# Optimization experiments

Measured on AMD Instinct MI355X. Metric: run time of the kernel, lower is better.

Reference implementation:

```python
import jax, jax.numpy as jnp
import numpy as np

BIG_CONST = 1000000.0
LN_EPS = 1e-5

B, S, D = 2, 1024, 1024
N, H = 16, D // 16            # n_head, d_head
POS_LEN = 2 * S - 1


def setup_inputs() -> dict:
    key = jax.random.key(0)
    ks = jax.random.split(key, 16)
    std_qkv = np.sqrt(1.0 / float(D + N * H))   # EinsumLayer init: 1/sqrt(fan_in+fan_out)
    std_post = np.sqrt(1.0 / float(N * H + D))
    return {
        "q": jax.random.normal(ks[0], (B, S, D), jnp.float32),
        "k": jax.random.normal(ks[1], (B, S, D), jnp.float32),
        "v": jax.random.normal(ks[2], (B, S, D), jnp.float32),
        "pos_enc": jax.random.normal(ks[3], (POS_LEN, D), jnp.float32),
        "attn_mask": jax.random.randint(ks[4], (B, 1, 1, S), 0, 2, jnp.int32),
        "q_w": jax.random.normal(ks[5], (D, N, H), jnp.float32) * std_qkv,
        "k_w": jax.random.normal(ks[6], (D, N, H), jnp.float32) * std_qkv,
        "k_b": jnp.zeros((N, H), jnp.float32),
        "v_w": jax.random.normal(ks[7], (D, N, H), jnp.float32) * std_qkv,
        "v_b": jnp.zeros((N, H), jnp.float32),
        "r_w_bias": jax.random.uniform(ks[8], (N, 1, H), jnp.float32, 0.0, 0.1),
        "r_r_bias": jax.random.uniform(ks[9], (N, 1, H), jnp.float32, 0.0, 0.1),
        "r_kernel": jax.random.uniform(ks[10], (N, D, H), jnp.float32, 0.0, 0.1),
        "post_w": jax.random.normal(ks[11], (N, H, D), jnp.float32) * std_post,
        "post_b": jnp.zeros((D,), jnp.float32),
        "ln_g": jnp.ones((D,), jnp.float32),
        "ln_b": jnp.zeros((D,), jnp.float32),
    }


def reference(q, k, v, pos_enc, attn_mask, q_w, k_w, k_b, v_w, v_b,
              r_w_bias, r_r_bias, r_kernel, post_w, post_b, ln_g, ln_b):
    input_q = q
    d_head = q_w.shape[-1]
    normalizer = 1.0 / np.sqrt(d_head)

    # head projections -> [B, N, L, H]
    qh = jnp.einsum('bld,dnh->bnlh', q, q_w)
    kh = jnp.einsum('bld,dnh->bnlh', k, k_w) + k_b[None, :, None, :] * 0 + jnp.transpose(k_b, (0, 1))[None, :, None, :] * 0 + k_b.reshape(1, k_b.shape[0], 1, k_b.shape[1])
    kh = jnp.einsum('bld,dnh->bnlh', k, k_w) + k_b.reshape(1, -1, 1, d_head)
    vh = jnp.einsum('bld,dnh->bnlh', v, v_w) + v_b.reshape(1, -1, 1, d_head)

    # content score: (q + r_w_bias) @ k^T * normalizer   [B,N,S,S]
    content = jnp.einsum('bnqh,bnkh->bnqk', qh + r_w_bias[None], kh) * normalizer

    # positional term (rel_shift with shift=0): r = pos_enc @ r_kernel -> [N, P, H]
    r = jnp.einsum('pd,ndh->nph', pos_enc, r_kernel)
    pos_scores = jnp.einsum('bnqh,nph->bnqp', qh + r_r_bias[None], r) * normalizer
    # shift=0 => reshape-swap + narrow + reshape-back is an exact identity; then narrow to k_len
    k_len = kh.shape[-2]
    pos_term = pos_scores[..., :k_len]

    attn_score = (content + pos_term).astype(jnp.float32)
    attn_score = attn_score - BIG_CONST * attn_mask.astype(jnp.float32)
    attn_dist = jax.nn.softmax(attn_score, axis=-1)

    out = jnp.einsum('bnqk,bnkh->bnqh', attn_dist, vh)          # [B,N,S,H]
    attn_out = jnp.einsum('bnlh,nhd->bld', out, post_w) + post_b

    x = input_q + attn_out
    mu = jnp.mean(x, axis=-1, keepdims=True)
    var = jnp.mean(jnp.square(x - mu), axis=-1, keepdims=True)
    return (x - mu) / jnp.sqrt(var + LN_EPS) * ln_g + ln_b
```

## Files before the change

### kernel.cpp

```cpp
#include <hip/hip_runtime.h>
#include <cstddef>
#include <cstdint>

typedef unsigned short u16;
typedef unsigned int   u32;

#define S_LEN  1024
#define NHEAD  16
#define HDIM   64
#define DMODEL 1024
#define NORMSC 0.125f
#define BIGC   1000000.0f
#define LOG2E  1.44269504088896f
#define SC2    (0.125f * 1.44269504088896f)

typedef __bf16 bf16x8 __attribute__((ext_vector_type(8)));
typedef float  f32x4  __attribute__((ext_vector_type(4)));

#define MFMA16(a, b, c) __builtin_amdgcn_mfma_f32_16x16x32_bf16((a), (b), (c), 0, 0, 0)

__device__ __forceinline__ u16 f2bf(float f) {
    u32 u = __float_as_uint(f);
    u32 r = (u + 0x7fffu + ((u >> 16) & 1u)) >> 16;
    return (u16)r;
}
__device__ __forceinline__ float bf2f(u32 v) {
    return __uint_as_float(v << 16);
}
__device__ __forceinline__ float4 unp4(uint2 u) {
    float4 f;
    f.x = bf2f(u.x & 0xffffu); f.y = bf2f(u.x >> 16);
    f.z = bf2f(u.y & 0xffffu); f.w = bf2f(u.y >> 16);
    return f;
}
__device__ __forceinline__ void async16(const void* g, void* l) {
    __builtin_amdgcn_global_load_lds(
        (__attribute__((address_space(1))) void*)(g),
        (__attribute__((address_space(3))) void*)(l), 16, 0, 0);
}

__global__ __launch_bounds__(256) void prep_all(
    const float* q, const float* k, const float* v, const float* pos,
    const float* qw, const float* kw, const float* vw, const float* pw, const float* rk,
    u16* qbf, u16* kbf, u16* vbf, u16* posb,
    u16* qwT, u16* kwT, u16* vwT, u16* pwT, u16* WrT)
{
    __shared__ float tb[32][33];
    const int bid = blockIdx.x, tid = threadIdx.x;
    if (bid < 7168) {
        const float* s; u16* d; int base;
        if (bid < 2048)      { s = q;   d = qbf;  base = bid; }
        else if (bid < 4096) { s = k;   d = kbf;  base = bid - 2048; }
        else if (bid < 6144) { s = v;   d = vbf;  base = bid - 4096; }
        else                 { s = pos; d = posb; base = bid - 6144; }
        const int i = base * 1024 + tid * 4;
        const float4 val = *(const float4*)&s[i];
        uint2 o;
        o.x = (u32)f2bf(val.x) | ((u32)f2bf(val.y) << 16);
        o.y = (u32)f2bf(val.z) | ((u32)f2bf(val.w) << 16);
        *(uint2*)&d[i] = o;
        return;
    }
    const int t = bid - 7168;
    const float* in; u16* out; int ild, r0, c0;
    if (t < 4096) {
        const int ts = t & 1023;
        if (t < 1024)      { in = qw; out = qwT; }
        else if (t < 2048) { in = kw; out = kwT; }
        else if (t < 3072) { in = vw; out = vwT; }
        else               { in = pw; out = pwT; }
        ild = 1024;
        r0 = (ts >> 5) * 32; c0 = (ts & 31) * 32;
    } else {
        const int ts = t - 4096;
        const int n = ts >> 6, tt = ts & 63;
        in = rk + (size_t)n * 65536; out = WrT + (size_t)n * 65536;
        ild = 64;
        r0 = (tt >> 1) * 32; c0 = (tt & 1) * 32;
    }
    const int tx = tid & 31, ty = tid >> 5;
    for (int i = ty; i < 32; i += 8)
        tb[i][tx] = in[(size_t)(r0 + i) * ild + c0 + tx];
    __syncthreads();
    for (int i = ty; i < 32; i += 8)
        out[(size_t)(c0 + i) * 1024 + r0 + tx] = f2bf(tb[tx][i]);
}

struct GJ { const u16* A; const u16* Bt; u16* C; int M; int k0; int klen; };

__global__ __launch_bounds__(256) void gemm_p(
    GJ j0, GJ j1, GJ j2, GJ j3, GJ j4, GJ j5, GJ j6, GJ j7)
{
    GJ g;
    switch (blockIdx.z) {
        case 0: g = j0; break; case 1: g = j1; break;
        case 2: g = j2; break; case 3: g = j3; break;
        case 4: g = j4; break; case 5: g = j5; break;
        case 6: g = j6; break; default: g = j7;
    }
    const int bm = blockIdx.y * 128;
    if (bm >= g.M) return;
    const int bn = blockIdx.x * 128;
    __shared__ u16 As[2][4096];
    __shared__ u16 Bs[2][4096];
    const int tid = threadIdx.x;
    const int w = tid >> 6, lane = tid & 63;
    const int wm = (w >> 1) * 64, wn = (w & 1) * 64;
    const int l15 = lane & 15, l16 = lane >> 4;
    f32x4 acc[4][4] = {};
    const char* Ab = (const char*)g.A;
    const char* Bb = (const char*)g.Bt;
    const int kend = g.k0 + g.klen;
    const int m0 = w * 1024 + lane * 16;
    const int m1 = (4 + w) * 1024 + lane * 16;
    const int r0w = m0 >> 6, cb0 = m0 & 63;
    const int r1w = m1 >> 6, cb1 = m1 & 63;
    async16(Ab + ((size_t)(bm + r0w) * 1024 + g.k0) * 2 + cb0, (char*)As[0] + m0);
    async16(Bb + ((size_t)(bn + r0w) * 1024 + g.k0) * 2 + cb0, (char*)Bs[0] + m0);
    async16(Ab + ((size_t)(bm + r1w) * 1024 + g.k0) * 2 + cb1, (char*)As[0] + m1);
    async16(Bb + ((size_t)(bn + r1w) * 1024 + g.k0) * 2 + cb1, (char*)Bs[0] + m1);
    int buf = 0;
    for (int k0 = g.k0; k0 < kend; k0 += 32) {
        __syncthreads();
        const int kn = k0 + 32;
        if (kn < kend) {
            async16(Ab + ((size_t)(bm + r0w) * 1024 + kn) * 2 + cb0, (char*)As[buf ^ 1] + m0);
            async16(Bb + ((size_t)(bn + r0w) * 1024 + kn) * 2 + cb0, (char*)Bs[buf ^ 1] + m0);
            async16(Ab + ((size_t)(bm + r1w) * 1024 + kn) * 2 + cb1, (char*)As[buf ^ 1] + m1);
            async16(Bb + ((size_t)(bn + r1w) * 1024 + kn) * 2 + cb1, (char*)Bs[buf ^ 1] + m1);
        }
        bf16x8 af[4], bfr[4];
#pragma unroll
        for (int i = 0; i < 4; ++i)
            af[i] = *(const bf16x8*)&As[buf][(wm + i * 16 + l15) * 32 + l16 * 8];
#pragma unroll
        for (int j = 0; j < 4; ++j)
            bfr[j] = *(const bf16x8*)&Bs[buf][(wn + j * 16 + l15) * 32 + l16 * 8];
#pragma unroll
        for (int i = 0; i < 4; ++i)
#pragma unroll
            for (int j = 0; j < 4; ++j)
                acc[i][j] = MFMA16(af[i], bfr[j], acc[i][j]);
        buf ^= 1;
    }
#pragma unroll
    for (int i = 0; i < 4; ++i)
#pragma unroll
        for (int j = 0; j < 4; ++j) {
            const int c = bn + wn + j * 16 + l15;
#pragma unroll
            for (int rg = 0; rg < 4; ++rg) {
                const int m = bm + wm + i * 16 + l16 * 4 + rg;
                g.C[(size_t)m * 1024 + c] = f2bf(acc[i][j][rg]);
            }
        }
}

__global__ __launch_bounds__(256) void prep2(
    const u16* pk0, const u16* pk1, const u16* pr0, const u16* pr1,
    const u16* pv0, const u16* pv1, const u16* pq0, const u16* pq1,
    const float* kbi, const float* vbi, const float* rwb, const float* rrb,
    const int* mask, u16* keff, float* cc, u16* vT, u16* qhb)
{
    __shared__ float tb[32][33];
    const int bid = blockIdx.x, tid = threadIdx.x;
    if (bid < 2048) {
        const int t = bid * 256 + tid;
        const int row = t >> 4, li = t & 15;
        const int n = (row >> 10) & 15, kk = row & 1023, b = row >> 14;
        const size_t mi = ((size_t)(b * 1024 + kk)) * 1024 + n * 64 + li * 4;
        const size_t pi = ((size_t)kk) * 1024 + n * 64 + li * 4;
        const float4 k0v = unp4(*(const uint2*)&pk0[mi]);
        const float4 k1v = unp4(*(const uint2*)&pk1[mi]);
        const float4 r0v = unp4(*(const uint2*)&pr0[pi]);
        const float4 r1v = unp4(*(const uint2*)&pr1[pi]);
        const float4 kb4 = *(const float4*)&kbi[n * 64 + li * 4];
        float4 kv, rv;
        kv.x = k0v.x + k1v.x + kb4.x; kv.y = k0v.y + k1v.y + kb4.y;
        kv.z = k0v.z + k1v.z + kb4.z; kv.w = k0v.w + k1v.w + kb4.w;
        rv.x = r0v.x + r1v.x; rv.y = r0v.y + r1v.y;
        rv.z = r0v.z + r1v.z; rv.w = r0v.w + r1v.w;
        const float4 w1 = *(const float4*)&rwb[n * 64 + li * 4];
        const float4 w2 = *(const float4*)&rrb[n * 64 + li * 4];
        float s = w1.x * kv.x + w1.y * kv.y + w1.z * kv.z + w1.w * kv.w
                + w2.x * rv.x + w2.y * rv.y + w2.z * rv.z + w2.w * rv.w;
        uint2 o;
        o.x = (u32)f2bf(kv.x + rv.x) | ((u32)f2bf(kv.y + rv.y) << 16);
        o.y = (u32)f2bf(kv.z + rv.z) | ((u32)f2bf(kv.w + rv.w) << 16);
        *(uint2*)&keff[(size_t)row * 64 + li * 4] = o;
#pragma unroll
        for (int m = 1; m < 16; m <<= 1) s += __shfl_xor(s, m);
        if (li == 0)
            cc[row] = LOG2E * (NORMSC * s - BIGC * (float)mask[b * 1024 + kk]);
        return;
    }
    if (bid < 4096) {
        const int t = bid - 2048;
        const int head = t >> 6, tt = t & 63;
        const int b = head >> 4, n = head & 15;
        const int r0 = (tt >> 1) * 32, c0 = (tt & 1) * 32;
        const int tx = tid & 31, ty = tid >> 5;
        const float vb = vbi[n * 64 + c0 + tx];
        for (int i = ty; i < 32; i += 8) {
            const size_t idx = ((size_t)(b * 1024 + r0 + i)) * 1024 + n * 64 + c0 + tx;
            tb[i][tx] = bf2f(pv0[idx]) + bf2f(pv1[idx]) + vb;
        }
        __syncthreads();
        u16* out = vT + (size_t)head * 65536;
        for (int i = ty; i < 32; i += 8)
            out[(size_t)(c0 + i) * 1024 + r0 + tx] = f2bf(tb[tx][i]);
        return;
    }
    const int t = bid - 4096;
    const int e = t * 1024 + tid * 4;
    const int m = e >> 10, c = e & 1023;
    const float4 a = unp4(*(const uint2*)&pq0[e]);
    const float4 b4 = unp4(*(const uint2*)&pq1[e]);
    uint2 o;
    o.x = (u32)f2bf(a.x + b4.x) | ((u32)f2bf(a.y + b4.y) << 16);
    o.y = (u32)f2bf(a.z + b4.z) | ((u32)f2bf(a.w + b4.w) << 16);
    const int b2 = m >> 10, l = m & 1023, n = c >> 6, h = c & 63;
    *(uint2*)&qhb[(((size_t)(b2 * NHEAD + n)) * 1024 + l) * 64 + h] = o;
}

__global__ __launch_bounds__(128) void attn_mfma(
    const u16* qb, const u16* kb, const u16* vtb, const float* ccomb, u16* O)
{
    __shared__ u16   Ks[2][4096];
    __shared__ u16   Vs[2][4096];
    __shared__ __bf16 Ps[2][1024];
    const int tid = threadIdx.x;
    const int w = tid >> 6, lane = tid & 63;
    const int l15 = lane & 15, l16 = lane >> 4;
    const int head = blockIdx.x >> 5;
    const int q0 = (blockIdx.x & 31) * 32;
    const int b = head >> 4, n = head & 15;
    const size_t hoff = (size_t)head * 65536;
    const u16* qh = qb + hoff;
    const char* khc = (const char*)(kb + hoff);
    const char* vtc = (const char*)(vtb + hoff);
    const float* cc = ccomb + head * 1024;
    __bf16* Pw = Ps[w];

    bf16x8 qf[2];
    {
        const size_t rb = ((size_t)(q0 + w * 16 + l15)) * 64 + l16 * 8;
        qf[0] = *(const bf16x8*)&qh[rb];
        qf[1] = *(const bf16x8*)&qh[rb + 32];
    }
    f32x4 Oacc[4] = {};
    float lsum[4] = {};

    const int sr0 = w * 32 + (lane >> 3);
    const int sc0 = lane & 7;
#pragma unroll
    for (int i = 0; i < 4; ++i) {
        const int r = sr0 + i * 8;
        async16(khc + r * 128 + (((sc0 + r) & 7) << 4), (char*)Ks[0] + r * 128 + sc0 * 16);
        async16(vtc + (size_t)r * 2048 + (((sc0 + r) & 7) << 4), (char*)Vs[0] + r * 128 + sc0 * 16);
    }
    int buf = 0;
    for (int kc = 0; kc < 16; ++kc) {
        __syncthreads();
        if (kc < 15) {
            const int kn = kc + 1;
#pragma unroll
            for (int i = 0; i < 4; ++i) {
                const int r = sr0 + i * 8;
                async16(khc + kn * 8192 + r * 128 + (((sc0 + r) & 7) << 4),
                        (char*)Ks[buf ^ 1] + r * 128 + sc0 * 16);
                async16(vtc + (size_t)r * 2048 + kn * 128 + (((sc0 + r) & 7) << 4),
                        (char*)Vs[buf ^ 1] + r * 128 + sc0 * 16);
            }
        }
        const u16* Kb = Ks[buf];
        const u16* Vb = Vs[buf];
        f32x4 sc[4];
#pragma unroll
        for (int j = 0; j < 4; ++j) {
            const int rk2 = j * 16 + l15;
            const int base = rk2 * 64;
            f32x4 a = {0.f, 0.f, 0.f, 0.f};
            a = MFMA16(qf[0], *(const bf16x8*)&Kb[base + (((l16 - rk2) & 7) << 3)], a);
            a = MFMA16(qf[1], *(const bf16x8*)&Kb[base + (((l16 + 4 - rk2) & 7) << 3)], a);
            const float cadd = cc[kc * 64 + j * 16 + l15];
            sc[j] = a * SC2 + cadd;
        }
#pragma unroll
        for (int j = 0; j < 4; ++j) {
            const int cg = j * 2 + (l15 >> 3);
#pragma unroll
            for (int rg = 0; rg < 4; ++rg) {
                const float p = exp2f(sc[j][rg]);
                lsum[rg] += p;
                const int row = l16 * 4 + rg;
                Pw[row * 64 + (((cg - row) & 7) << 3) + (l15 & 7)] = (__bf16)p;
            }
        }
        bf16x8 pf[2];
#pragma unroll
        for (int f = 0; f < 2; ++f)
            pf[f] = *(const bf16x8*)&Pw[l15 * 64 + (((f * 4 + l16 - l15) & 7) << 3)];
#pragma unroll
        for (int t4 = 0; t4 < 4; ++t4) {
#pragma unroll
            for (int f = 0; f < 2; ++f) {
                const int vr = t4 * 16 + l15;
                const int ch = f * 4 + l16;
                const bf16x8 vf = *(const bf16x8*)&Vb[vr * 64 + (((ch - vr) & 7) << 3)];
                Oacc[t4] = MFMA16(pf[f], vf, Oacc[t4]);
            }
        }
        buf ^= 1;
    }
    float inv[4];
#pragma unroll
    for (int rg = 0; rg < 4; ++rg) {
        float s = lsum[rg];
#pragma unroll
        for (int m = 1; m < 16; m <<= 1) s += __shfl_xor(s, m);
        inv[rg] = 1.0f / s;
    }
#pragma unroll
    for (int t4 = 0; t4 < 4; ++t4) {
#pragma unroll
        for (int rg = 0; rg < 4; ++rg) {
            const int srow = q0 + w * 16 + l16 * 4 + rg;
            const int col = n * 64 + t4 * 16 + l15;
            O[((size_t)b * 1024 + srow) * 1024 + col] = f2bf(Oacc[t4][rg] * inv[rg]);
        }
    }
}

__global__ __launch_bounds__(256) void ln_kernel(
    const u16* __restrict__ p0, const u16* __restrict__ p1,
    const u16* __restrict__ p2, const u16* __restrict__ p3,
    const float* __restrict__ resid, const float* __restrict__ pb,
    const float* __restrict__ g, const float* __restrict__ bb,
    float* __restrict__ out)
{
    const int row = blockIdx.x;
    const int tid = threadIdx.x;
    const size_t i = (size_t)row * DMODEL + tid * 4;
    const float4 a0 = unp4(*(const uint2*)&p0[i]);
    const float4 a1 = unp4(*(const uint2*)&p1[i]);
    const float4 a2 = unp4(*(const uint2*)&p2[i]);
    const float4 a3 = unp4(*(const uint2*)&p3[i]);
    const float4 rr = *(const float4*)&resid[i];
    const float4 pv = *(const float4*)&pb[tid * 4];
    float4 v;
    v.x = a0.x + a1.x + a2.x + a3.x + rr.x + pv.x;
    v.y = a0.y + a1.y + a2.y + a3.y + rr.y + pv.y;
    v.z = a0.z + a1.z + a2.z + a3.z + rr.z + pv.z;
    v.w = a0.w + a1.w + a2.w + a3.w + rr.w + pv.w;
    float s1 = v.x + v.y + v.z + v.w;
    float s2 = v.x * v.x + v.y * v.y + v.z * v.z + v.w * v.w;
#pragma unroll
    for (int off = 32; off; off >>= 1) {
        s1 += __shfl_down(s1, off);
        s2 += __shfl_down(s2, off);
    }
    __shared__ float rb[8];
    if ((tid & 63) == 0) { rb[tid >> 6] = s1; rb[4 + (tid >> 6)] = s2; }
    __syncthreads();
    if (tid == 0) {
        rb[0] = rb[0] + rb[1] + rb[2] + rb[3];
        rb[4] = rb[4] + rb[5] + rb[6] + rb[7];
    }
    __syncthreads();
    s1 = rb[0]; s2 = rb[4];
    const float mu = s1 * (1.0f / DMODEL);
    const float var = s2 * (1.0f / DMODEL) - mu * mu;
    const float rstd = rsqrtf(var + 1e-5f);
    const float4 gv = *(const float4*)&g[tid * 4];
    const float4 bv = *(const float4*)&bb[tid * 4];
    float4 o;
    o.x = (v.x - mu) * rstd * gv.x + bv.x;
    o.y = (v.y - mu) * rstd * gv.y + bv.y;
    o.z = (v.z - mu) * rstd * gv.z + bv.z;
    o.w = (v.w - mu) * rstd * gv.w + bv.w;
    *(float4*)&out[i] = o;
}

extern "C" void kernel_launch(void* const* d_in, const int* in_sizes, int n_in,
                              void* d_out, int out_size, void* d_ws, size_t ws_size,
                              hipStream_t stream)
{
    (void)in_sizes; (void)n_in; (void)out_size; (void)ws_size;
    const float* q   = (const float*)d_in[0];
    const float* k   = (const float*)d_in[1];
    const float* v   = (const float*)d_in[2];
    const float* pos = (const float*)d_in[3];
    const int*   msk = (const int*)d_in[4];
    const float* qw  = (const float*)d_in[5];
    const float* kw  = (const float*)d_in[6];
    const float* kbi = (const float*)d_in[7];
    const float* vw  = (const float*)d_in[8];
    const float* vbi = (const float*)d_in[9];
    const float* rwb = (const float*)d_in[10];
    const float* rrb = (const float*)d_in[11];
    const float* rk  = (const float*)d_in[12];
    const float* pw  = (const float*)d_in[13];
    const float* pb  = (const float*)d_in[14];
    const float* lg  = (const float*)d_in[15];
    const float* lb  = (const float*)d_in[16];
    float* out = (float*)d_out;

    float* fb = (float*)d_ws;
    float* cc   = fb;
    u16* us   = (u16*)(cc + 32768);
    u16* qbf  = us;
    u16* kbf  = qbf + 2097152;
    u16* vbf  = kbf + 2097152;
    u16* posb = vbf + 2097152;
    u16* qwT  = posb + 1048576;
    u16* kwT  = qwT + 1048576;
    u16* vwT  = kwT + 1048576;
    u16* pwT  = vwT + 1048576;
    u16* WrT  = pwT + 1048576;
    u16* qhb  = WrT + 1048576;
    u16* keffb= qhb + 2097152;
    u16* vTb  = keffb + 2097152;
    u16* pq0  = vTb + 2097152;
    u16* pq1  = pq0 + 2097152;
    u16* pk0  = pq1 + 2097152;
    u16* pk1  = pk0 + 2097152;
    u16* pv0  = pk1 + 2097152;
    u16* pv1  = pv0 + 2097152;
    u16* pr0  = pv1 + 2097152;
    u16* pr1  = pr0 + 1048576;
    u16* po0  = pr1 + 1048576;
    u16* po1  = po0 + 2097152;
    u16* po2  = po1 + 2097152;
    u16* po3  = po2 + 2097152;
    u16* Obf  = qbf;

    dim3 blk(256);
    prep_all<<<12288, blk, 0, stream>>>(q, k, v, pos, qw, kw, vw, pw, rk,
                                        qbf, kbf, vbf, posb, qwT, kwT, vwT, pwT, WrT);

    GJ jq0 = {qbf,  qwT, pq0, 2048, 0,   512};
    GJ jq1 = {qbf,  qwT, pq1, 2048, 512, 512};
    GJ jk0 = {kbf,  kwT, pk0, 2048, 0,   512};
    GJ jk1 = {kbf,  kwT, pk1, 2048, 512, 512};
    GJ jv0 = {vbf,  vwT, pv0, 2048, 0,   512};
    GJ jv1 = {vbf,  vwT, pv1, 2048, 512, 512};
    GJ jp0 = {posb, WrT, pr0, 1024, 0,   512};
    GJ jp1 = {posb, WrT, pr1, 1024, 512, 512};
    gemm_p<<<dim3(8, 16, 8), blk, 0, stream>>>(jq0, jq1, jk0, jk1, jv0, jv1, jp0, jp1);

    prep2<<<6144, blk, 0, stream>>>(pk0, pk1, pr0, pr1, pv0, pv1, pq0, pq1,
                                    kbi, vbi, rwb, rrb, msk, keffb, cc, vTb, qhb);

    attn_mfma<<<1024, dim3(128), 0, stream>>>(qhb, keffb, vTb, cc, Obf);

    GJ jo0 = {Obf, pwT, po0, 2048, 0,   256};
    GJ jo1 = {Obf, pwT, po1, 2048, 256, 256};
    GJ jo2 = {Obf, pwT, po2, 2048, 512, 256};
    GJ jo3 = {Obf, pwT, po3, 2048, 768, 256};
    gemm_p<<<dim3(8, 16, 4), blk, 0, stream>>>(jo0, jo1, jo2, jo3, jo0, jo0, jo0, jo0);

    ln_kernel<<<2048, blk, 0, stream>>>(po0, po1, po2, po3, q, pb, lg, lb, out);
}
```

Baseline: 212.8 us.

## Swizzle GEMM LDS tiles and remap block indices for XCD-local reuse

Rotates 16-byte chunks within each row of the GEMM shared-memory tiles, with a matching rotated read offset, to remove LDS bank conflicts on the MFMA fragment loads. It also flattens the GEMM and attention grids to 1D and remaps block IDs so that blocks sharing the same job or head tend to land on the same XCD, aiming for better L2 reuse on MI355X. The costs are extra index arithmetic and a swizzle that must stay consistent between the async writes and the fragment reads.

After: 203.3 us. -4.5%, faster.

```diff
diff --git a/kernel.cpp b/kernel.cpp
--- a/kernel.cpp
+++ b/kernel.cpp
@@ -89,18 +89,24 @@
 struct GJ { const u16* A; const u16* Bt; u16* C; int M; int k0; int klen; };
 
 __global__ __launch_bounds__(256) void gemm_p(
-    GJ j0, GJ j1, GJ j2, GJ j3, GJ j4, GJ j5, GJ j6, GJ j7)
-{
+    GJ j0, GJ j1, GJ j2, GJ j3, GJ j4, GJ j5, GJ j6, GJ j7, int nj)
+{
+    const int bid = blockIdx.x;
+    const int c8 = bid & 7;
+    const int x = (bid >> 3) & 7;
+    int z, y;
+    if (nj == 8) { z = c8; y = bid >> 6; }
+    else         { z = c8 >> 1; y = ((c8 & 1) << 3) + (bid >> 6); }
     GJ g;
-    switch (blockIdx.z) {
+    switch (z) {
         case 0: g = j0; break; case 1: g = j1; break;
         case 2: g = j2; break; case 3: g = j3; break;
         case 4: g = j4; break; case 5: g = j5; break;
         case 6: g = j6; break; default: g = j7;
     }
-    const int bm = blockIdx.y * 128;
+    const int bm = y * 128;
     if (bm >= g.M) return;
-    const int bn = blockIdx.x * 128;
+    const int bn = x * 128;
     __shared__ u16 As[2][4096];
     __shared__ u16 Bs[2][4096];
     const int tid = threadIdx.x;
@@ -113,29 +119,30 @@
     const int kend = g.k0 + g.klen;
     const int m0 = w * 1024 + lane * 16;
     const int m1 = (4 + w) * 1024 + lane * 16;
-    const int r0w = m0 >> 6, cb0 = m0 & 63;
-    const int r1w = m1 >> 6, cb1 = m1 & 63;
-    async16(Ab + ((size_t)(bm + r0w) * 1024 + g.k0) * 2 + cb0, (char*)As[0] + m0);
-    async16(Bb + ((size_t)(bn + r0w) * 1024 + g.k0) * 2 + cb0, (char*)Bs[0] + m0);
-    async16(Ab + ((size_t)(bm + r1w) * 1024 + g.k0) * 2 + cb1, (char*)As[0] + m1);
-    async16(Bb + ((size_t)(bn + r1w) * 1024 + g.k0) * 2 + cb1, (char*)Bs[0] + m1);
+    const int r0w = m0 >> 6, rc0 = ((((m0 >> 4) & 3) + r0w) & 3) << 4;
+    const int r1w = m1 >> 6, rc1 = ((((m1 >> 4) & 3) + r1w) & 3) << 4;
+    async16(Ab + ((size_t)(bm + r0w) * 1024 + g.k0) * 2 + rc0, (char*)As[0] + m0);
+    async16(Bb + ((size_t)(bn + r0w) * 1024 + g.k0) * 2 + rc0, (char*)Bs[0] + m0);
+    async16(Ab + ((size_t)(bm + r1w) * 1024 + g.k0) * 2 + rc1, (char*)As[0] + m1);
+    async16(Bb + ((size_t)(bn + r1w) * 1024 + g.k0) * 2 + rc1, (char*)Bs[0] + m1);
+    const int rotA = ((l16 - l15) & 3) << 3;
     int buf = 0;
     for (int k0 = g.k0; k0 < kend; k0 += 32) {
         __syncthreads();
         const int kn = k0 + 32;
         if (kn < kend) {
-            async16(Ab + ((size_t)(bm + r0w) * 1024 + kn) * 2 + cb0, (char*)As[buf ^ 1] + m0);
-            async16(Bb + ((size_t)(bn + r0w) * 1024 + kn) * 2 + cb0, (char*)Bs[buf ^ 1] + m0);
-            async16(Ab + ((size_t)(bm + r1w) * 1024 + kn) * 2 + cb1, (char*)As[buf ^ 1] + m1);
-            async16(Bb + ((size_t)(bn + r1w) * 1024 + kn) * 2 + cb1, (char*)Bs[buf ^ 1] + m1);
+            async16(Ab + ((size_t)(bm + r0w) * 1024 + kn) * 2 + rc0, (char*)As[buf ^ 1] + m0);
+            async16(Bb + ((size_t)(bn + r0w) * 1024 + kn) * 2 + rc0, (char*)Bs[buf ^ 1] + m0);
+            async16(Ab + ((size_t)(bm + r1w) * 1024 + kn) * 2 + rc1, (char*)As[buf ^ 1] + m1);
+            async16(Bb + ((size_t)(bn + r1w) * 1024 + kn) * 2 + rc1, (char*)Bs[buf ^ 1] + m1);
         }
         bf16x8 af[4], bfr[4];
 #pragma unroll
         for (int i = 0; i < 4; ++i)
-            af[i] = *(const bf16x8*)&As[buf][(wm + i * 16 + l15) * 32 + l16 * 8];
+            af[i] = *(const bf16x8*)&As[buf][(wm + i * 16 + l15) * 32 + rotA];
 #pragma unroll
         for (int j = 0; j < 4; ++j)
-            bfr[j] = *(const bf16x8*)&Bs[buf][(wn + j * 16 + l15) * 32 + l16 * 8];
+            bfr[j] = *(const bf16x8*)&Bs[buf][(wn + j * 16 + l15) * 32 + rotA];
 #pragma unroll
         for (int i = 0; i < 4; ++i)
 #pragma unroll
@@ -232,8 +239,10 @@
     const int tid = threadIdx.x;
     const int w = tid >> 6, lane = tid & 63;
     const int l15 = lane & 15, l16 = lane >> 4;
-    const int head = blockIdx.x >> 5;
-    const int q0 = (blockIdx.x & 31) * 32;
+    const int bid = blockIdx.x;
+    const int i128 = bid >> 3;
+    const int head = (bid & 7) * 4 + (i128 >> 5);
+    const int q0 = (i128 & 31) * 32;
     const int b = head >> 4, n = head & 15;
     const size_t hoff = (size_t)head * 65536;
     const u16* qh = qb + hoff;
@@ -447,7 +456,7 @@
     GJ jv1 = {vbf,  vwT, pv1, 2048, 512, 512};
     GJ jp0 = {posb, WrT, pr0, 1024, 0,   512};
     GJ jp1 = {posb, WrT, pr1, 1024, 512, 512};
-    gemm_p<<<dim3(8, 16, 8), blk, 0, stream>>>(jq0, jq1, jk0, jk1, jv0, jv1, jp0, jp1);
+    gemm_p<<<1024, blk, 0, stream>>>(jq0, jq1, jk0, jk1, jv0, jv1, jp0, jp1, 8);
 
     prep2<<<6144, blk, 0, stream>>>(pk0, pk1, pr0, pr1, pv0, pv1, pq0, pq1,
                                     kbi, vbi, rwb, rrb, msk, keffb, cc, vTb, qhb);
@@ -458,7 +467,7 @@
     GJ jo1 = {Obf, pwT, po1, 2048, 256, 256};
     GJ jo2 = {Obf, pwT, po2, 2048, 512, 256};
     GJ jo3 = {Obf, pwT, po3, 2048, 768, 256};
-    gemm_p<<<dim3(8, 16, 4), blk, 0, stream>>>(jo0, jo1, jo2, jo3, jo0, jo0, jo0, jo0);
+    gemm_p<<<512, blk, 0, stream>>>(jo0, jo1, jo2, jo3, jo0, jo0, jo0, jo0, 4);
 
     ln_kernel<<<2048, blk, 0, stream>>>(po0, po1, po2, po3, q, pb, lg, lb, out);
 }
```
